# Kernel tuning notes

Hardware: AMD Instinct MI355X
Metric: run time of the kernel (lower is better)

The kernel has to match this reference:

```python
import jax, jax.numpy as jnp
import numpy as np

N_HEADS = 16
HEAD_DIM = 64  # dim=1024 / n_heads=16


def setup_inputs() -> dict:
    key = jax.random.key(0)
    ks = jax.random.split(key, 7)
    B, S, D = 4, 2048, 1024
    scale = 1.0 / np.sqrt(D)
    return {
        "q": jax.random.normal(ks[0], (B, S, D), jnp.float32),
        "k": jax.random.normal(ks[1], (B, S, D), jnp.float32),
        "v": jax.random.normal(ks[2], (B, S, D), jnp.float32),
        "Wq": jax.random.normal(ks[3], (D, D), jnp.float32) * scale,
        "Wk": jax.random.normal(ks[4], (D, D), jnp.float32) * scale,
        "Wv": jax.random.normal(ks[5], (D, D), jnp.float32) * scale,
        "Wo": jax.random.normal(ks[6], (D, D), jnp.float32) * scale,
    }


def reference(q, k, v, Wq, Wk, Wv, Wo):
    B, S, _ = q.shape
    H, Dh = N_HEADS, HEAD_DIM
    # linear projections (torch Linear: x @ W.T), reshape to [B, H, S, Dh]
    xq = (q @ Wq.T).reshape(B, S, H, Dh).transpose(0, 2, 1, 3)
    xk = (k @ Wk.T).reshape(B, S, H, Dh).transpose(0, 2, 1, 3)
    xv = (v @ Wv.T).reshape(B, S, H, Dh).transpose(0, 2, 1, 3)
    scores = jnp.einsum("bhsd,bhtd->bhst", xq, xk) / jnp.sqrt(jnp.float32(Dh))
    # causal mask: -inf above diagonal
    causal = jnp.triu(jnp.full((S, S), -jnp.inf, jnp.float32), k=1)
    scores = scores + causal[None, None]
    attn = jax.nn.softmax(scores.astype(jnp.float32), axis=-1).astype(xq.dtype)
    out = jnp.einsum("bhst,bhtd->bhsd", attn, xv)
    out = out.transpose(0, 2, 1, 3).reshape(B, S, H * Dh)
    return out @ Wo.T
```

## Files before the change

kernel.cpp:

```cpp
#include <hip/hip_runtime.h>
#include <hip/hip_bf16.h>

#define DI __device__ __forceinline__

typedef __attribute__((ext_vector_type(8))) short short8;
typedef __attribute__((ext_vector_type(4))) short short4v;
typedef __attribute__((ext_vector_type(4))) float f32x4;

#define QSCALE 0.180336885f

DI short f2bf(float f) {
  __hip_bfloat16 h = __float2bfloat16(f);
  return __builtin_bit_cast(short, h);
}

DI float fexp2(float x) {
#if __has_builtin(__builtin_amdgcn_exp2f)
  return __builtin_amdgcn_exp2f(x);
#else
  return exp2f(x);
#endif
}

DI void gl16(const short* g, short* l) {
  __builtin_amdgcn_global_load_lds(
      (const __attribute__((address_space(1))) void*)g,
      (__attribute__((address_space(3))) void*)l, 16, 0, 0);
}

__global__ __launch_bounds__(256) void convert_all(
    const float* __restrict__ q, const float* __restrict__ k,
    const float* __restrict__ v, const float* __restrict__ wq,
    const float* __restrict__ wk, const float* __restrict__ wv,
    const float* __restrict__ wo, short* __restrict__ qb,
    short* __restrict__ kb, short* __restrict__ vb, short* __restrict__ wb) {
  int z = blockIdx.z;
  const float* src;
  short* dst;
  if (z < 3) {
    src = (z == 0) ? q : (z == 1) ? k : v;
    dst = (z == 0) ? qb : (z == 1) ? kb : vb;
  } else {
    if (blockIdx.x >= 512) return;
    src = (z == 3) ? wq : (z == 4) ? wk : (z == 5) ? wv : wo;
    dst = wb + (size_t)(z - 3) * 1024 * 1024;
  }
  size_t i = ((size_t)blockIdx.x * 256 + threadIdx.x) * 8;
  float4 f0 = *(const float4*)(src + i);
  float4 f1 = *(const float4*)(src + i + 4);
  short8 o;
  o[0] = f2bf(f0.x); o[1] = f2bf(f0.y); o[2] = f2bf(f0.z); o[3] = f2bf(f0.w);
  o[4] = f2bf(f1.x); o[5] = f2bf(f1.y); o[6] = f2bf(f1.z); o[7] = f2bf(f1.w);
  *(short8*)(dst + i) = o;
}

__global__ __launch_bounds__(256) void convert_one(
    const float* __restrict__ src, short* __restrict__ dst) {
  size_t i = ((size_t)blockIdx.x * 256 + threadIdx.x) * 8;
  float4 f0 = *(const float4*)(src + i);
  float4 f1 = *(const float4*)(src + i + 4);
  short8 o;
  o[0] = f2bf(f0.x); o[1] = f2bf(f0.y); o[2] = f2bf(f0.z); o[3] = f2bf(f0.w);
  o[4] = f2bf(f1.x); o[5] = f2bf(f1.y); o[6] = f2bf(f1.z); o[7] = f2bf(f1.w);
  *(short8*)(dst + i) = o;
}

enum { OUT_F32 = 0, OUT_HEAD = 1, OUT_HEADT = 2 };

DI void stage_tile(const short* __restrict__ A, const short* __restrict__ B,
                   short* dA, short* dB, int bm, int bn, int k0, int wid,
                   int lrr, int lch) {
#pragma unroll
  for (int i = 0; i < 4; ++i) {
    int r0 = wid * 32 + i * 8;
    int rr = r0 + lrr;
    int sc = (lch ^ (rr & 7)) << 3;
    gl16(A + (size_t)(bm + rr) * 1024 + k0 + sc, dA + r0 * 64);
    gl16(B + (size_t)(bn + rr) * 1024 + k0 + sc, dB + r0 * 64);
  }
}

template <int OMODE>
DI void gemm_core(short* sA, short* sB, const short* __restrict__ A,
                  const short* __restrict__ B, void* __restrict__ Cp,
                  float scale, int bm, int bn) {
  const int tid = threadIdx.x;
  const int lane = tid & 63;
  const int wid = tid >> 6;
  const int wm = wid >> 1, wn = wid & 1;
  const int l15 = lane & 15, lq = lane >> 4;
  const int lrr = lane >> 3;
  const int lch = lane & 7;

  f32x4 acc[4][4] = {};

  stage_tile(A, B, sA, sB, bm, bn, 0, wid, lrr, lch);

  int cur = 0;
  for (int t = 0; t < 16; ++t) {
    if (t < 15) {
      stage_tile(A, B, sA + (cur ^ 1) * 8192, sB + (cur ^ 1) * 8192, bm, bn,
                 (t + 1) * 64, wid, lrr, lch);
      asm volatile("s_waitcnt vmcnt(8)" ::: "memory");
    } else {
      asm volatile("s_waitcnt vmcnt(0)" ::: "memory");
    }
    __builtin_amdgcn_s_barrier();

    const char* bA = (const char*)(sA + cur * 8192);
    const char* bB = (const char*)(sB + cur * 8192);
#pragma unroll
    for (int ks = 0; ks < 2; ++ks) {
      short8 a[4], b[4];
#pragma unroll
      for (int mt = 0; mt < 4; ++mt) {
        int row = wm * 64 + mt * 16 + l15;
        int off = (row * 128 + ks * 64 + lq * 16) ^ ((row & 7) << 4);
        a[mt] = *(const short8*)(bA + off);
      }
#pragma unroll
      for (int nt = 0; nt < 4; ++nt) {
        int row = wn * 64 + nt * 16 + l15;
        int off = (row * 128 + ks * 64 + lq * 16) ^ ((row & 7) << 4);
        b[nt] = *(const short8*)(bB + off);
      }
#pragma unroll
      for (int mt = 0; mt < 4; ++mt)
#pragma unroll
        for (int nt = 0; nt < 4; ++nt) {
          if (OMODE == OUT_HEADT)
            acc[mt][nt] = __builtin_amdgcn_mfma_f32_16x16x32_bf16(
                b[nt], a[mt], acc[mt][nt], 0, 0, 0);
          else
            acc[mt][nt] = __builtin_amdgcn_mfma_f32_16x16x32_bf16(
                a[mt], b[nt], acc[mt][nt], 0, 0, 0);
        }
    }
    __builtin_amdgcn_s_barrier();
    cur ^= 1;
  }

#pragma unroll
  for (int mt = 0; mt < 4; ++mt) {
#pragma unroll
    for (int nt = 0; nt < 4; ++nt) {
#pragma unroll
      for (int r = 0; r < 4; ++r) {
        float val = acc[mt][nt][r] * scale;
        if (OMODE == OUT_HEADT) {
          int f = bn + wn * 64 + nt * 16 + lq * 4 + r;
          int t = bm + wm * 64 + mt * 16 + l15;
          int bb = t >> 11, s = t & 2047;
          int h = f >> 6, dh = f & 63;
          ((short*)Cp)[((size_t)((bb * 16 + h) * 64 + dh)) * 2048 + s] = f2bf(val);
        } else {
          int rowg = bm + wm * 64 + mt * 16 + lq * 4 + r;
          int colg = bn + wn * 64 + nt * 16 + l15;
          if (OMODE == OUT_HEAD) {
            int bb = rowg >> 11, s = rowg & 2047;
            int h = colg >> 6, dh = colg & 63;
            ((short*)Cp)[((size_t)(bb * 16 + h) * 2048 + s) * 64 + dh] = f2bf(val);
          } else {
            ((float*)Cp)[(size_t)rowg * 1024 + colg] = val;
          }
        }
      }
    }
  }
}

DI void xcd_map(int id, int& bm, int& bn) {
  int xcd = id & 7, slot = id >> 3;
  int panel = xcd + 8 * (slot >> 3);
  int ntile = slot & 7;
  bm = panel * 128;
  bn = ntile * 128;
}

#define GEMM_LDS()                                  \
  __shared__ __align__(16) short sA[2 * 128 * 64];  \
  __shared__ __align__(16) short sB[2 * 128 * 64];

__global__ __launch_bounds__(256) void proj_gemm3(
    const short* __restrict__ qb, const short* __restrict__ kb,
    const short* __restrict__ vb, const short* __restrict__ wq,
    const short* __restrict__ wk, const short* __restrict__ wv,
    short* __restrict__ xq, short* __restrict__ xk, short* __restrict__ xvT) {
  GEMM_LDS();
  int z = blockIdx.z;
  int bm, bn;
  xcd_map(blockIdx.x, bm, bn);
  if (z == 0) {
    gemm_core<OUT_HEAD>(sA, sB, qb, wq, xq, QSCALE, bm, bn);
  } else if (z == 1) {
    gemm_core<OUT_HEAD>(sA, sB, kb, wk, xk, 1.0f, bm, bn);
  } else {
    gemm_core<OUT_HEADT>(sA, sB, vb, wv, xvT, 1.0f, bm, bn);
  }
}

__global__ __launch_bounds__(256) void proj_oneN(
    const short* __restrict__ A, const short* __restrict__ B,
    short* __restrict__ C, float scale) {
  GEMM_LDS();
  int bm, bn;
  xcd_map(blockIdx.x, bm, bn);
  gemm_core<OUT_HEAD>(sA, sB, A, B, C, scale, bm, bn);
}

__global__ __launch_bounds__(256) void proj_oneT(
    const short* __restrict__ A, const short* __restrict__ B,
    short* __restrict__ C, float scale) {
  GEMM_LDS();
  int bm, bn;
  xcd_map(blockIdx.x, bm, bn);
  gemm_core<OUT_HEADT>(sA, sB, A, B, C, scale, bm, bn);
}

__global__ __launch_bounds__(256) void final_gemm(
    const short* __restrict__ oa, const short* __restrict__ wo,
    float* __restrict__ out) {
  GEMM_LDS();
  int bm, bn;
  xcd_map(blockIdx.x, bm, bn);
  gemm_core<OUT_F32>(sA, sB, oa, wo, out, 1.0f, bm, bn);
}

__global__ __launch_bounds__(512, 4) void attn_k(
    const short* __restrict__ Xq, const short* __restrict__ Xk,
    const short* __restrict__ XvT, short* __restrict__ Oa) {
  __shared__ __align__(16) short sK[2][64 * 64];
  __shared__ __align__(16) short sVT[2][64 * 64];
  __shared__ __align__(16) short sP[8][16 * 64];

  const int tid = threadIdx.x;
  const int lane = tid & 63;
  const int wid = tid >> 6;
  const int l15 = lane & 15, lq = lane >> 4;
  const int bid = blockIdx.x;
  const int ipair = bid >> 6;
  const int bh = bid & 63;
  const int b = bh >> 4, h = bh & 15;

  const short* Q = Xq + (size_t)bh * 2048 * 64;
  const short* K = Xk + (size_t)bh * 2048 * 64;
  const short* VT = XvT + (size_t)bh * 64 * 2048;

  const int srow = tid >> 3;
  const int scol = (tid & 7) * 8;
  const int soff = (srow * 128 + scol * 2) ^ ((srow & 7) << 4);

  short8 kreg, vreg;
  kreg = *(const short8*)(K + (size_t)srow * 64 + scol);
  vreg = *(const short8*)(VT + (size_t)srow * 2048 + scol);

  *(short8*)((char*)sK[0] + soff) = kreg;
  *(short8*)((char*)sVT[0] + soff) = vreg;

  short* sPw = sP[wid];
  int p = 0;

  for (int seg = 0; seg < 2; ++seg) {
    const int qt = seg ? ipair : (15 - ipair);
    const int qfirst = qt * 128 + wid * 16;
    const int qg = qfirst + l15;
    const int qlast = qfirst + 15;
    const int ntile = 2 * qt + 2;

    short8 qf[2];
#pragma unroll
    for (int ks = 0; ks < 2; ++ks)
      qf[ks] = *(const short8*)(Q + (size_t)qg * 64 + ks * 32 + lq * 8);

    float m_run = -1e30f, l_run = 0.f;
    f32x4 acc[4] = {};

    for (int kt = 0; kt < ntile; ++kt) {
      const int kv0 = kt * 64;
      __syncthreads();

      int nkt = kt + 1, nseg = seg;
      if (nkt >= ntile) { nseg = seg + 1; nkt = 0; }
      const bool hn = (nseg < 2);
      if (hn) {
        const int kn = nkt * 64;
        kreg = *(const short8*)(K + (size_t)(kn + srow) * 64 + scol);
        vreg = *(const short8*)(VT + (size_t)srow * 2048 + kn + scol);
      }

      const bool fullmask = (kv0 > qlast);
      if (!fullmask) {
        const bool needmask = (kv0 + 63 > qfirst);
        const char* bufK = (const char*)sK[p];
        const char* bufV = (const char*)sVT[p];

        f32x4 sc[4] = {};
        __builtin_amdgcn_s_setprio(1);
#pragma unroll
        for (int ks = 0; ks < 2; ++ks) {
          short8 kf[4];
#pragma unroll
          for (int nt = 0; nt < 4; ++nt) {
            int row = nt * 16 + l15;
            int off = (row * 128 + ks * 64 + lq * 16) ^ ((row & 7) << 4);
            kf[nt] = *(const short8*)(bufK + off);
          }
#pragma unroll
          for (int nt = 0; nt < 4; ++nt)
            sc[nt] = __builtin_amdgcn_mfma_f32_16x16x32_bf16(kf[nt], qf[ks],
                                                             sc[nt], 0, 0, 0);
        }
        __builtin_amdgcn_s_setprio(0);

        float pv[4][4];
        float m = -1e30f;
        if (needmask) {
#pragma unroll
          for (int nt = 0; nt < 4; ++nt)
#pragma unroll
            for (int r = 0; r < 4; ++r) {
              float s = sc[nt][r];
              if (kv0 + nt * 16 + lq * 4 + r > qg) s = -1e30f;
              pv[nt][r] = s;
              m = fmaxf(m, s);
            }
        } else {
#pragma unroll
          for (int nt = 0; nt < 4; ++nt)
#pragma unroll
            for (int r = 0; r < 4; ++r) {
              float s = sc[nt][r];
              pv[nt][r] = s;
              m = fmaxf(m, s);
            }
        }
        m = fmaxf(m, __shfl_xor(m, 16));
        m = fmaxf(m, __shfl_xor(m, 32));

        if (!__all(m - m_run <= 8.0f)) {
          const float m_new = fmaxf(m_run, m);
          const float corr = fexp2(m_run - m_new);
          l_run *= corr;
#pragma unroll
          for (int mt = 0; mt < 4; ++mt)
#pragma unroll
            for (int r = 0; r < 4; ++r) acc[mt][r] *= corr;
          m_run = m_new;
        }

        float rsum = 0.f;
#pragma unroll
        for (int nt = 0; nt < 4; ++nt)
#pragma unroll
          for (int r = 0; r < 4; ++r) {
            float e = fexp2(pv[nt][r] - m_run);
            pv[nt][r] = e;
            rsum += e;
          }
        rsum += __shfl_xor(rsum, 16);
        rsum += __shfl_xor(rsum, 32);
        l_run += rsum;

#pragma unroll
        for (int nt = 0; nt < 4; ++nt) {
          short4v pw;
#pragma unroll
          for (int r = 0; r < 4; ++r) pw[r] = f2bf(pv[nt][r]);
          int off = (l15 * 128 + nt * 32 + lq * 8) ^ ((l15 & 7) << 4);
          *(short4v*)((char*)sPw + off) = pw;
        }

        __builtin_amdgcn_s_setprio(1);
#pragma unroll
        for (int ks = 0; ks < 2; ++ks) {
          int poff = (l15 * 128 + ks * 64 + lq * 16) ^ ((l15 & 7) << 4);
          short8 pf = *(const short8*)((const char*)sPw + poff);
#pragma unroll
          for (int mt = 0; mt < 4; ++mt) {
            int row = mt * 16 + l15;
            int voff = (row * 128 + ks * 64 + lq * 16) ^ ((row & 7) << 4);
            short8 vf = *(const short8*)(bufV + voff);
            acc[mt] = __builtin_amdgcn_mfma_f32_16x16x32_bf16(vf, pf, acc[mt],
                                                              0, 0, 0);
          }
        }
        __builtin_amdgcn_s_setprio(0);
      }

      if (hn) {
        *(short8*)((char*)sK[p ^ 1] + soff) = kreg;
        *(short8*)((char*)sVT[p ^ 1] + soff) = vreg;
      }
      p ^= 1;
    }

    const float rl = 1.0f / l_run;
    short* orow = Oa + ((size_t)(b * 2048 + qg)) * 1024 + h * 64;
#pragma unroll
    for (int mt = 0; mt < 4; ++mt) {
      short4v o;
#pragma unroll
      for (int r = 0; r < 4; ++r) o[r] = f2bf(acc[mt][r] * rl);
      *(short4v*)(orow + mt * 16 + lq * 4) = o;
    }
  }
}

extern "C" void kernel_launch(void* const* d_in, const int* in_sizes, int n_in,
                              void* d_out, int out_size, void* d_ws,
                              size_t ws_size, hipStream_t stream) {
  const float* q = (const float*)d_in[0];
  const float* k = (const float*)d_in[1];
  const float* v = (const float*)d_in[2];
  const float* Wq = (const float*)d_in[3];
  const float* Wk = (const float*)d_in[4];
  const float* Wv = (const float*)d_in[5];
  const float* Wo = (const float*)d_in[6];

  char* ws = (char*)d_ws;
  short* wq_b = (short*)(ws + (0ull << 20));
  short* wk_b = (short*)(ws + (2ull << 20));
  short* wv_b = (short*)(ws + (4ull << 20));
  short* wo_b = (short*)(ws + (6ull << 20));
  short* xq  = (short*)(ws + (8ull << 20));
  short* xk  = (short*)(ws + (24ull << 20));
  short* xvT = (short*)(ws + (56ull << 20));

  if (ws_size >= (122ull << 20)) {
    short* qb = (short*)(ws + (72ull << 20));
    short* kb = (short*)(ws + (88ull << 20));
    short* vb = (short*)(ws + (104ull << 20));
    short* oa = qb;

    convert_all<<<dim3(4096, 1, 7), 256, 0, stream>>>(q, k, v, Wq, Wk, Wv, Wo,
                                                      qb, kb, vb, wq_b);
    proj_gemm3<<<dim3(512, 1, 3), 256, 0, stream>>>(qb, kb, vb, wq_b, wk_b,
                                                    wv_b, xq, xk, xvT);
    attn_k<<<dim3(512), 512, 0, stream>>>(xq, xk, xvT, oa);
    final_gemm<<<dim3(512), 256, 0, stream>>>(oa, wo_b, (float*)d_out);
  } else {
    short* X = (short*)(ws + (8ull << 20));
    short* xq2 = (short*)(ws + (24ull << 20));
    short* xk2 = (short*)(ws + (40ull << 20));
    short* xvT2 = (short*)(ws + (56ull << 20));
    short* oa2 = (short*)(ws + (72ull << 20));

    convert_one<<<dim3(512), 256, 0, stream>>>(Wq, wq_b);
    convert_one<<<dim3(512), 256, 0, stream>>>(Wk, wk_b);
    convert_one<<<dim3(512), 256, 0, stream>>>(Wv, wv_b);
    convert_one<<<dim3(512), 256, 0, stream>>>(Wo, wo_b);
    convert_one<<<dim3(4096), 256, 0, stream>>>(q, X);
    proj_oneN<<<dim3(512), 256, 0, stream>>>(X, wq_b, xq2, QSCALE);
    convert_one<<<dim3(4096), 256, 0, stream>>>(k, X);
    proj_oneN<<<dim3(512), 256, 0, stream>>>(X, wk_b, xk2, 1.0f);
    convert_one<<<dim3(4096), 256, 0, stream>>>(v, X);
    proj_oneT<<<dim3(512), 256, 0, stream>>>(X, wv_b, xvT2, 1.0f);
    attn_k<<<dim3(512), 512, 0, stream>>>(xq2, xk2, xvT2, oa2);
    final_gemm<<<dim3(512), 256, 0, stream>>>(oa2, wo_b, (float*)d_out);
  }
}
```

Before: 174.2 us.

## Replace QKV projection GEMM with 256x256-tile, 8-wave pipelined kernel

Replaces the 128x128-tile fused QKV projection kernel with a new 256x256-tile kernel that uses 512 threads and one block per CU. Global-to-LDS staging of the next K-slices is interleaved across four MFMA quarter phases, with split barriers and s_setprio around the MFMA bursts. The larger tile raises arithmetic intensity and cuts redundant global loads. In exchange it uses more LDS and registers per block and launches only 384 blocks, which risks wave-quantization and occupancy problems.

```diff
diff --git a/kernel.cpp b/kernel.cpp
--- a/kernel.cpp
+++ b/kernel.cpp
@@ -66,6 +66,152 @@
 }
 
 enum { OUT_F32 = 0, OUT_HEAD = 1, OUT_HEADT = 2 };
+
+DI void stage_half(const short* __restrict__ g, short* lds, int bmn, int k0,
+                   int half, int wid_, int lrr, int lch) {
+  int r0 = half * 128 + wid_ * 8;
+#pragma unroll
+  for (int i = 0; i < 2; ++i) {
+    int rb = r0 + i * 64;
+    int rr = rb + lrr;
+    int sc = (lch ^ (rr & 7)) << 3;
+    gl16(g + (size_t)(bmn + rr) * 1024 + k0 + sc, lds + rb * 64);
+  }
+}
+
+template <int OMODE, int Q>
+DI void do_quad(const char* bufA, const short8 (&bfr)[4][2],
+                f32x4 (&acc)[8][4], int wm, int l15, int lq) {
+  short8 afr[2][2];
+#pragma unroll
+  for (int i = 0; i < 2; ++i)
+#pragma unroll
+    for (int ks = 0; ks < 2; ++ks) {
+      int row = wm * 128 + (Q * 2 + i) * 16 + l15;
+      int off = (row * 128 + ks * 64 + lq * 16) ^ ((row & 7) << 4);
+      afr[i][ks] = *(const short8*)(bufA + off);
+    }
+  __builtin_amdgcn_s_setprio(1);
+#pragma unroll
+  for (int i = 0; i < 2; ++i)
+#pragma unroll
+    for (int nt = 0; nt < 4; ++nt)
+#pragma unroll
+      for (int ks = 0; ks < 2; ++ks) {
+        if (OMODE == OUT_HEADT)
+          acc[Q * 2 + i][nt] = __builtin_amdgcn_mfma_f32_16x16x32_bf16(
+              bfr[nt][ks], afr[i][ks], acc[Q * 2 + i][nt], 0, 0, 0);
+        else
+          acc[Q * 2 + i][nt] = __builtin_amdgcn_mfma_f32_16x16x32_bf16(
+              afr[i][ks], bfr[nt][ks], acc[Q * 2 + i][nt], 0, 0, 0);
+      }
+  __builtin_amdgcn_s_setprio(0);
+}
+
+template <int OMODE>
+DI void gemm256_core(short* sA, short* sB, const short* __restrict__ A,
+                     const short* __restrict__ B, void* __restrict__ Cp,
+                     float scale, int bm, int bn) {
+  const int tid = threadIdx.x;
+  const int lane = tid & 63;
+  const int wid = tid >> 6;
+  const int wm = wid >> 2, wn = wid & 3;
+  const int l15 = lane & 15, lq = lane >> 4;
+  const int lrr = lane >> 3, lch = lane & 7;
+
+  f32x4 acc[8][4] = {};
+
+  stage_half(A, sA, bm, 0, 0, wid, lrr, lch);
+  stage_half(A, sA, bm, 0, 1, wid, lrr, lch);
+  stage_half(B, sB, bn, 0, 0, wid, lrr, lch);
+  stage_half(B, sB, bn, 0, 1, wid, lrr, lch);
+  stage_half(A, sA + 16384, bm, 64, 0, wid, lrr, lch);
+  stage_half(A, sA + 16384, bm, 64, 1, wid, lrr, lch);
+  stage_half(B, sB + 16384, bn, 64, 0, wid, lrr, lch);
+  stage_half(B, sB + 16384, bn, 64, 1, wid, lrr, lch);
+  asm volatile("s_waitcnt vmcnt(8)" ::: "memory");
+  __builtin_amdgcn_s_barrier();
+
+  for (int k = 0; k < 16; ++k) {
+    const char* bufA = (const char*)(sA + (k & 1) * 16384);
+    const char* bufB = (const char*)(sB + (k & 1) * 16384);
+    short* stA = sA + ((k + 1) & 1) * 16384;
+    short* stB = sB + (k & 1) * 16384;
+    const bool stgA = (k >= 1 && k < 15);
+    const bool stgB = (k < 14);
+
+    short8 bfr[4][2];
+    if (stgA) stage_half(A, stA, bm, (k + 1) * 64, 0, wid, lrr, lch);
+#pragma unroll
+    for (int nt = 0; nt < 4; ++nt)
+#pragma unroll
+      for (int ks = 0; ks < 2; ++ks) {
+        int row = wn * 64 + nt * 16 + l15;
+        int off = (row * 128 + ks * 64 + lq * 16) ^ ((row & 7) << 4);
+        bfr[nt][ks] = *(const short8*)(bufB + off);
+      }
+    do_quad<OMODE, 0>(bufA, bfr, acc, wm, l15, lq);
+    __builtin_amdgcn_s_barrier();
+    if (stgA) stage_half(A, stA, bm, (k + 1) * 64, 1, wid, lrr, lch);
+    if (stgB) stage_half(B, stB, bn, (k + 2) * 64, 0, wid, lrr, lch);
+    do_quad<OMODE, 1>(bufA, bfr, acc, wm, l15, lq);
+    __builtin_amdgcn_s_barrier();
+    if (stgB) stage_half(B, stB, bn, (k + 2) * 64, 1, wid, lrr, lch);
+    do_quad<OMODE, 2>(bufA, bfr, acc, wm, l15, lq);
+    __builtin_amdgcn_s_barrier();
+    do_quad<OMODE, 3>(bufA, bfr, acc, wm, l15, lq);
+    if (k < 14) {
+      asm volatile("s_waitcnt vmcnt(4)" ::: "memory");
+      __builtin_amdgcn_s_barrier();
+    } else if (k == 14) {
+      asm volatile("s_waitcnt vmcnt(0)" ::: "memory");
+      __builtin_amdgcn_s_barrier();
+    }
+  }
+
+#pragma unroll
+  for (int mt = 0; mt < 8; ++mt)
+#pragma unroll
+    for (int nt = 0; nt < 4; ++nt)
+#pragma unroll
+      for (int r = 0; r < 4; ++r) {
+        float val = acc[mt][nt][r] * scale;
+        if (OMODE == OUT_HEADT) {
+          int f = bn + wn * 64 + nt * 16 + lq * 4 + r;
+          int t = bm + wm * 128 + mt * 16 + l15;
+          int bb = t >> 11, s = t & 2047;
+          int h = f >> 6, dh = f & 63;
+          ((short*)Cp)[((size_t)((bb * 16 + h) * 64 + dh)) * 2048 + s] = f2bf(val);
+        } else {
+          int rowg = bm + wm * 128 + mt * 16 + lq * 4 + r;
+          int colg = bn + wn * 64 + nt * 16 + l15;
+          int bb = rowg >> 11, s = rowg & 2047;
+          int h = colg >> 6, dh = colg & 63;
+          ((short*)Cp)[((size_t)(bb * 16 + h) * 2048 + s) * 64 + dh] = f2bf(val);
+        }
+      }
+}
+
+__global__ __launch_bounds__(512, 1) void proj_gemm256(
+    const short* __restrict__ qb, const short* __restrict__ kb,
+    const short* __restrict__ vb, const short* __restrict__ wq,
+    const short* __restrict__ wk, const short* __restrict__ wv,
+    short* __restrict__ xq, short* __restrict__ xk, short* __restrict__ xvT) {
+  __shared__ __align__(16) short sA[2 * 256 * 64];
+  __shared__ __align__(16) short sB[2 * 256 * 64];
+  int gid = blockIdx.x;
+  int xcd = gid & 7, slot = gid >> 3;
+  int pg = xcd + 8 * (slot >> 2);
+  int ntile = slot & 3;
+  int z = pg >> 5, pm = pg & 31;
+  int bm = pm * 256, bn = ntile * 256;
+  if (z == 0)
+    gemm256_core<OUT_HEAD>(sA, sB, qb, wq, xq, QSCALE, bm, bn);
+  else if (z == 1)
+    gemm256_core<OUT_HEAD>(sA, sB, kb, wk, xk, 1.0f, bm, bn);
+  else
+    gemm256_core<OUT_HEADT>(sA, sB, vb, wv, xvT, 1.0f, bm, bn);
+}
 
 DI void stage_tile(const short* __restrict__ A, const short* __restrict__ B,
                    short* dA, short* dB, int bm, int bn, int k0, int wid,
@@ -181,24 +327,6 @@
   __shared__ __align__(16) short sA[2 * 128 * 64];  \
   __shared__ __align__(16) short sB[2 * 128 * 64];
 
-__global__ __launch_bounds__(256) void proj_gemm3(
-    const short* __restrict__ qb, const short* __restrict__ kb,
-    const short* __restrict__ vb, const short* __restrict__ wq,
-    const short* __restrict__ wk, const short* __restrict__ wv,
-    short* __restrict__ xq, short* __restrict__ xk, short* __restrict__ xvT) {
-  GEMM_LDS();
-  int z = blockIdx.z;
-  int bm, bn;
-  xcd_map(blockIdx.x, bm, bn);
-  if (z == 0) {
-    gemm_core<OUT_HEAD>(sA, sB, qb, wq, xq, QSCALE, bm, bn);
-  } else if (z == 1) {
-    gemm_core<OUT_HEAD>(sA, sB, kb, wk, xk, 1.0f, bm, bn);
-  } else {
-    gemm_core<OUT_HEADT>(sA, sB, vb, wv, xvT, 1.0f, bm, bn);
-  }
-}
-
 __global__ __launch_bounds__(256) void proj_oneN(
     const short* __restrict__ A, const short* __restrict__ B,
     short* __restrict__ C, float scale) {
@@ -434,8 +562,8 @@
 
     convert_all<<<dim3(4096, 1, 7), 256, 0, stream>>>(q, k, v, Wq, Wk, Wv, Wo,
                                                       qb, kb, vb, wq_b);
-    proj_gemm3<<<dim3(512, 1, 3), 256, 0, stream>>>(qb, kb, vb, wq_b, wk_b,
-                                                    wv_b, xq, xk, xvT);
+    proj_gemm256<<<dim3(384), 512, 0, stream>>>(qb, kb, vb, wq_b, wk_b, wv_b,
+                                                xq, xk, xvT);
     attn_k<<<dim3(512), 512, 0, stream>>>(xq, xk, xvT, oa);
     final_gemm<<<dim3(512), 256, 0, stream>>>(oa, wo_b, (float*)d_out);
   } else {
```

Measured after the change: 191.7 us. +10.1%, slower.
